# Performance work log

Hardware: AMD Instinct MI355X
Metric: run time of the kernel (lower is better)

The kernel has to match this reference:

```python
import jax, jax.numpy as jnp
import numpy as np

K = 3  # kernel_size
KK = K * K


def conv2d(x, w, b, stride=1, padding=1, dilation=1):
    out = jax.lax.conv_general_dilated(
        x, w, (stride, stride), [(padding, padding), (padding, padding)],
        rhs_dilation=(dilation, dilation),
        dimension_numbers=('NCHW', 'OIHW', 'NCHW'))
    return out + b[None, :, None, None]


def bilinear_gather(x, py, px):
    # x: [B,C,H,W]; py,px: [B,KK,H,W] float sampling coords (zero outside).
    B, C, H, W = x.shape
    y0 = jnp.floor(py)
    x0 = jnp.floor(px)
    wy1 = py - y0
    wx1 = px - x0
    xf = x.reshape(B, C, H * W)

    def corner(yc, xc, wgt):
        valid = (yc >= 0) & (yc <= H - 1) & (xc >= 0) & (xc <= W - 1)
        yi = jnp.clip(yc, 0, H - 1).astype(jnp.int32)
        xi = jnp.clip(xc, 0, W - 1).astype(jnp.int32)
        idx = (yi * W + xi).reshape(B, 1, -1)  # [B,1,KK*H*W]
        v = jnp.take_along_axis(xf, jnp.broadcast_to(idx, (B, C, idx.shape[-1])), axis=2)
        v = v.reshape(B, C, *yc.shape[1:])  # [B,C,KK,H,W]
        return v * (wgt * valid)[:, None]

    return (corner(y0, x0, (1 - wy1) * (1 - wx1)) +
            corner(y0, x0 + 1, (1 - wy1) * wx1) +
            corner(y0 + 1, x0, wy1 * (1 - wx1)) +
            corner(y0 + 1, x0 + 1, wy1 * wx1))


def modulated_deform_conv(x, offset, mask, w, b, stride=1, padding=1, dilation=1):
    B, C, H, W = x.shape
    Ho, Wo = offset.shape[2], offset.shape[3]
    off = offset.reshape(B, KK, 2, Ho, Wo)
    dy, dx = off[:, :, 0], off[:, :, 1]  # [B,KK,Ho,Wo]
    ki, kj = jnp.meshgrid(jnp.arange(K), jnp.arange(K), indexing='ij')
    ki = ki.reshape(-1).astype(x.dtype)  # [KK]
    kj = kj.reshape(-1).astype(x.dtype)
    base_y = (jnp.arange(Ho) * stride - padding).astype(x.dtype)
    base_x = (jnp.arange(Wo) * stride - padding).astype(x.dtype)
    py = base_y[None, None, :, None] + (ki * dilation)[None, :, None, None] + dy
    px = base_x[None, None, None, :] + (kj * dilation)[None, :, None, None] + dx
    x_off = bilinear_gather(x, py, px)              # [B,C,KK,Ho,Wo]
    x_off = x_off * mask[:, None]                   # modulation
    w_flat = w.reshape(w.shape[0], C, KK)           # [O,C,KK]
    out = jnp.einsum('bckhw,ock->bohw', x_off, w_flat)
    return out + b[None, :, None, None]


def setup_inputs() -> dict:
    key = jax.random.key(0)
    ks = jax.random.split(key, 7)
    B, C, O, H, W = 8, 64, 64, 128, 128
    x = jax.random.normal(ks[0], (B, C, H, W), dtype=jnp.float32)
    # offset/mask predictor convs (zero-init in the module; randomized small here
    # so offsets/masks are non-trivial for kernel correctness testing)
    p_w = jax.random.normal(ks[1], (2 * KK, C, 3, 3), dtype=jnp.float32) * 0.02
    p_b = jax.random.normal(ks[2], (2 * KK,), dtype=jnp.float32) * 0.1
    m_w = jax.random.normal(ks[3], (KK, C, 3, 3), dtype=jnp.float32) * 0.02
    m_b = jax.random.normal(ks[4], (KK,), dtype=jnp.float32) * 0.1
    # deformable conv weights
    d_w = jax.random.normal(ks[5], (O, C, K, K), dtype=jnp.float32) * (1.0 / np.sqrt(C * KK))
    d_b = jax.random.normal(ks[6], (O,), dtype=jnp.float32) * 0.01
    return {"x": x, "p_w": p_w, "p_b": p_b, "m_w": m_w, "m_b": m_b, "d_w": d_w, "d_b": d_b}


def reference(x, p_w, p_b, m_w, m_b, d_w, d_b):
    offset = conv2d(x, p_w, p_b, stride=1, padding=1, dilation=1)   # [B,18,H,W]
    mask = jax.nn.sigmoid(conv2d(x, m_w, m_b, stride=1, padding=1, dilation=1))  # [B,9,H,W]
    out = modulated_deform_conv(x, offset, mask, d_w, d_b, stride=1, padding=1, dilation=1)
    return (out, offset)
```

## Files before the change

### kernel.cpp

```cpp
#include <hip/hip_runtime.h>
#include <math.h>

#define KK 9
#define BB 8
#define CC 64
#define OO 64
#define HH 128
#define WW 128
#define HWSZ (HH*WW)

typedef _Float16 half8 __attribute__((ext_vector_type(8)));
typedef float    floatx4 __attribute__((ext_vector_type(4)));

#define WP_ELEMS (9*2*4*32*8)
#define WD_ELEMS (9*2*4*64*8)
#define XH_ELEMS ((size_t)BB*HWSZ*64)
#define NCONV 2048

__global__ __launch_bounds__(256) void prep(
    const float* __restrict__ x,
    const float* __restrict__ p_w, const float* __restrict__ m_w,
    const float* __restrict__ d_w,
    _Float16* __restrict__ Wp, _Float16* __restrict__ Wd, _Float16* __restrict__ x_h,
    int conv_blocks)
{
    const int blk = blockIdx.x;
    const int tid = threadIdx.x;
    if (blk < conv_blocks) {
        __shared__ _Float16 sh[64][72];
        const int b    = blk >> 8;
        const int pix0 = (blk & 255) * 64;
        const float* xb = x + (size_t)b*CC*HWSZ + pix0;
        {
            const int p     = tid & 63;
            const int cbase = tid >> 6;
            #pragma unroll
            for (int j = 0; j < 16; ++j) {
                const int c = j*4 + cbase;
                sh[p][c] = (_Float16)xb[(size_t)c*HWSZ + p];
            }
        }
        __syncthreads();
        {
            const int p  = tid >> 2;
            const int c0 = (tid & 3) * 16;
            _Float16* dst = x_h + ((size_t)b*HWSZ + pix0 + p)*64 + c0;
            *(half8*)dst       = *(const half8*)&sh[p][c0];
            *(half8*)(dst + 8) = *(const half8*)&sh[p][c0 + 8];
        }
    } else {
        const int i = (blk - conv_blocks)*256 + tid;
        if (i < WP_ELEMS) {
            const int e = i & 7, n = (i>>3)&31, quad = (i>>8)&3, ks = (i>>10)&1, k = i>>11;
            const int c = ks*32 + quad*8 + e;
            float v = 0.f;
            if (n < 18)      v = p_w[(n*CC + c)*KK + k];
            else if (n < 27) v = m_w[((n-18)*CC + c)*KK + k];
            Wp[i] = (_Float16)v;
        } else if (i < WP_ELEMS + WD_ELEMS) {
            const int j = i - WP_ELEMS;
            const int e = j & 7, o = (j>>3)&63, quad = (j>>9)&3, ks = (j>>11)&1, k = j>>12;
            const int c = ks*32 + quad*8 + e;
            Wd[j] = (_Float16)d_w[(o*CC + c)*KK + k];
        }
    }
}

__global__ __launch_bounds__(256, 6) void dcn_fused(
    const _Float16* __restrict__ x_h,
    const _Float16* __restrict__ Wp, const _Float16* __restrict__ Wd,
    const float* __restrict__ p_b, const float* __restrict__ m_b,
    const float* __restrict__ db,
    float* __restrict__ out, float* __restrict__ offset_out)
{
    __shared__ alignas(16) float T[27*68];

    const int tid  = threadIdx.x;
    const int wv   = tid >> 6;
    const int lane = tid & 63;
    const int quad = lane >> 4;
    const int l15  = lane & 15;
    const int b    = blockIdx.x & 7;
    const int seg  = blockIdx.x >> 3;
    const int row  = seg >> 1;
    const int col0 = (seg & 1) * 64;
    const int pix0 = row * WW + col0;
    const _Float16* xbh = x_h + (size_t)b*HWSZ*64;

    const int p2   = wv*16 + (lane >> 2);
    const int part = lane & 3;
    const int wx2  = col0 + p2;
    const int bidx = ((l15 << 2) | quad) << 2;

    union U { half8 h; int i[4]; };

    floatx4 accp[2];
    accp[0] = (floatx4)0.f; accp[1] = (floatx4)0.f;
    #pragma unroll
    for (int k = 0; k < 9; ++k) {
        const int hy = row + k/3 - 1;
        const int hx = wx2 + k%3 - 1;
        const bool vld = (hy >= 0) & (hy < HH) & (hx >= 0) & (hx < WW);
        const _Float16* ap = xbh + (size_t)(vld ? hy*WW + hx : 0)*64 + part*8;
        const half8 z = (half8)(_Float16)0.f;
        half8 a0 = *(const half8*)ap;
        half8 a1 = *(const half8*)(ap + 32);
        a0 = vld ? a0 : z;
        a1 = vld ? a1 : z;
        U u0, u1, b0, b1;
        u0.h = a0; u1.h = a1;
        #pragma unroll
        for (int d = 0; d < 4; ++d) {
            b0.i[d] = __builtin_amdgcn_ds_bpermute(bidx, u0.i[d]);
            b1.i[d] = __builtin_amdgcn_ds_bpermute(bidx, u1.i[d]);
        }
        const _Float16* wp = Wp + k*2048 + quad*256 + l15*8;
        accp[0] = __builtin_amdgcn_mfma_f32_16x16x32_f16(b0.h, *(const half8*)(wp),              accp[0], 0, 0, 0);
        accp[1] = __builtin_amdgcn_mfma_f32_16x16x32_f16(b0.h, *(const half8*)(wp + 128),        accp[1], 0, 0, 0);
        accp[0] = __builtin_amdgcn_mfma_f32_16x16x32_f16(b1.h, *(const half8*)(wp + 1024),       accp[0], 0, 0, 0);
        accp[1] = __builtin_amdgcn_mfma_f32_16x16x32_f16(b1.h, *(const half8*)(wp + 1024 + 128), accp[1], 0, 0, 0);
    }

    #pragma unroll
    for (int nt = 0; nt < 2; ++nt) {
        const int ch = nt*16 + l15;
        if (ch < 27) {
            const float bias = (ch < 18) ? p_b[ch] : m_b[ch-18];
            #pragma unroll
            for (int r = 0; r < 4; ++r)
                T[ch*68 + wv*16 + quad*4 + r] = accp[nt][r] + bias;
        }
    }
    __syncthreads();

    {
        float* offp = offset_out + (size_t)b*18*HWSZ + pix0;
        #pragma unroll
        for (int j = 0; j < 5; ++j) {
            const int idx = j*256 + tid;
            if (idx < 18*64) {
                const int ch = idx >> 6, pp = idx & 63;
                offp[ch*HWSZ + pp] = T[ch*68 + pp];
            }
        }
    }
    float dyk[9], dxk[9], mkk[9];
    #pragma unroll
    for (int k = 0; k < 9; ++k) {
        dyk[k] = T[(2*k  )*68 + p2];
        dxk[k] = T[(2*k+1)*68 + p2];
        mkk[k] = 1.f / (1.f + expf(-T[(18+k)*68 + p2]));
    }

    floatx4 acc[4];
    #pragma unroll
    for (int nt = 0; nt < 4; ++nt) acc[nt] = (floatx4)0.f;

    #pragma unroll
    for (int k = 0; k < 9; ++k) {
        const float dy = dyk[k], dx = dxk[k], mk = mkk[k];
        const float py  = (float)(row - 1 + k/3) + dy;
        const float pxf = (float)(wx2 - 1 + k%3) + dx;
        const float y0f = floorf(py), x0f = floorf(pxf);
        const int   iy0 = (int)y0f,   ix0 = (int)x0f;
        const float wy1 = py - y0f,   wx1 = pxf - x0f;
        const float wy0 = 1.f - wy1,  wx0 = 1.f - wx1;
        const bool vy0 = ((unsigned)iy0     < (unsigned)HH);
        const bool vy1 = ((unsigned)(iy0+1) < (unsigned)HH);
        const bool vx0 = ((unsigned)ix0     < (unsigned)WW);
        const bool vx1 = ((unsigned)(ix0+1) < (unsigned)WW);
        const int cy0 = min(max(iy0,   0), HH-1), cy1 = min(max(iy0+1, 0), HH-1);
        const int cx0 = min(max(ix0,   0), WW-1), cx1 = min(max(ix0+1, 0), WW-1);
        const int i0 = cy0*WW+cx0, i1 = cy0*WW+cx1, i2 = cy1*WW+cx0, i3 = cy1*WW+cx1;
        const _Float16 g0 = (_Float16)(wy0*wx0*((vy0&vx0) ? mk : 0.f));
        const _Float16 g1 = (_Float16)(wy0*wx1*((vy0&vx1) ? mk : 0.f));
        const _Float16 g2 = (_Float16)(wy1*wx0*((vy1&vx0) ? mk : 0.f));
        const _Float16 g3 = (_Float16)(wy1*wx1*((vy1&vx1) ? mk : 0.f));

        const _Float16* c0p = xbh + (size_t)i0*64 + part*8;
        const _Float16* c1p = xbh + (size_t)i1*64 + part*8;
        const _Float16* c2p = xbh + (size_t)i2*64 + part*8;
        const _Float16* c3p = xbh + (size_t)i3*64 + part*8;
        const half8 p0l = *(const half8*)c0p, p0h = *(const half8*)(c0p + 32);
        const half8 p1l = *(const half8*)c1p, p1h = *(const half8*)(c1p + 32);
        const half8 p2l = *(const half8*)c2p, p2h = *(const half8*)(c2p + 32);
        const half8 p3l = *(const half8*)c3p, p3h = *(const half8*)(c3p + 32);
        const half8 lo = p0l*g0 + p1l*g1 + p2l*g2 + p3l*g3;
        const half8 hi = p0h*g0 + p1h*g1 + p2h*g2 + p3h*g3;

        U ulo, uhi, a0u, a1u;
        ulo.h = lo; uhi.h = hi;
        #pragma unroll
        for (int d = 0; d < 4; ++d) {
            a0u.i[d] = __builtin_amdgcn_ds_bpermute(bidx, ulo.i[d]);
            a1u.i[d] = __builtin_amdgcn_ds_bpermute(bidx, uhi.i[d]);
        }

        #pragma unroll
        for (int ks = 0; ks < 2; ++ks) {
            const half8 af = ks ? a1u.h : a0u.h;
            const _Float16* wdp = Wd + k*4096 + ks*2048 + quad*512 + l15*8;
            #pragma unroll
            for (int nt = 0; nt < 4; ++nt)
                acc[nt] = __builtin_amdgcn_mfma_f32_16x16x32_f16(af, *(const half8*)(wdp + nt*128), acc[nt], 0, 0, 0);
        }
    }

    __syncthreads();
    float* T2 = T;
    #pragma unroll
    for (int oc = 0; oc < 4; ++oc) {
        #pragma unroll
        for (int r = 0; r < 4; ++r)
            T2[l15*68 + wv*16 + quad*4 + r] = acc[oc][r];
        __syncthreads();
        #pragma unroll
        for (int j = 0; j < 4; ++j) {
            const int idx = j*256 + tid;
            const int o16 = idx >> 6, pp = idx & 63;
            out[((size_t)b*OO + oc*16 + o16)*HWSZ + pix0 + pp] = T2[o16*68 + pp] + db[oc*16 + o16];
        }
        __syncthreads();
    }
}

__global__ __launch_bounds__(256, 4) void dcn_fused_lds(
    const float* __restrict__ x,
    const _Float16* __restrict__ Wp, const _Float16* __restrict__ Wd,
    const float* __restrict__ p_b, const float* __restrict__ m_b,
    const float* __restrict__ db,
    float* __restrict__ out, float* __restrict__ offset_out)
{
    __shared__ alignas(16) _Float16 A_sh[128][72];
    __shared__ alignas(16) _Float16 WM_sh[32*72];
    __shared__ alignas(16) _Float16 Wd_sh[64][72];

    const int tid   = threadIdx.x;
    const int wv    = tid >> 6;
    const int lane  = tid & 63;
    const int quad  = lane >> 4;
    const int l15   = lane & 15;
    const int b     = blockIdx.x & 7;
    const int row   = blockIdx.x >> 3;
    const int pix0  = row * WW;
    const int p     = tid & 127;
    const int chalf = (tid >> 7) * 32;
    const int h = row, w = p;
    const float* xb = x + (size_t)b*CC*HWSZ;
    _Float16 (*W_sh)[72] = (_Float16 (*)[72])WM_sh;

    floatx4 accp[2][2];
    #pragma unroll
    for (int mt = 0; mt < 2; ++mt)
        #pragma unroll
        for (int nt = 0; nt < 2; ++nt) accp[mt][nt] = (floatx4)0.f;

    for (int k = 0; k < 9; ++k) {
        {
            const int n  = tid >> 3;
            const int c0 = (tid & 7) * 8;
            *(half8*)&W_sh[n][c0] =
                *(const half8*)(Wp + k*2048 + (c0>>5)*1024 + ((c0>>3)&3)*256 + n*8);
        }
        const int hy = h + (k/3) - 1;
        const int wx = w + (k%3) - 1;
        const bool vld = (hy >= 0) & (hy < HH) & (wx >= 0) & (wx < WW);
        const float* xs = xb + hy*WW + wx;
        #pragma unroll
        for (int cb = 0; cb < 4; ++cb) {
            union { half8 v; _Float16 e[8]; } u;
            #pragma unroll
            for (int j = 0; j < 8; ++j)
                u.e[j] = (_Float16)(vld ? xs[(size_t)(chalf + cb*8 + j)*HWSZ] : 0.f);
            *(half8*)&A_sh[p][chalf + cb*8] = u.v;
        }
        __syncthreads();
        #pragma unroll
        for (int ks = 0; ks < 2; ++ks) {
            half8 bf[2];
            #pragma unroll
            for (int nt = 0; nt < 2; ++nt)
                bf[nt] = *(const half8*)&W_sh[nt*16 + l15][ks*32 + quad*8];
            #pragma unroll
            for (int mt = 0; mt < 2; ++mt) {
                half8 af = *(const half8*)&A_sh[wv*32 + mt*16 + l15][ks*32 + quad*8];
                accp[mt][0] = __builtin_amdgcn_mfma_f32_16x16x32_f16(af, bf[0], accp[mt][0], 0, 0, 0);
                accp[mt][1] = __builtin_amdgcn_mfma_f32_16x16x32_f16(af, bf[1], accp[mt][1], 0, 0, 0);
            }
        }
        __syncthreads();
    }

    float (*T)[132] = (float (*)[132])&A_sh[0][0];
    #pragma unroll
    for (int nt = 0; nt < 2; ++nt) {
        const int ch = nt*16 + l15;
        if (ch < 27) {
            #pragma unroll
            for (int mt = 0; mt < 2; ++mt)
                #pragma unroll
                for (int r = 0; r < 4; ++r)
                    T[ch][wv*32 + mt*16 + quad*4 + r] = accp[mt][nt][r];
        }
    }
    __syncthreads();

    float dyk[9], dxk[9], mkk[9];
    float* offp = offset_out + (size_t)b*18*HWSZ + pix0;
    #pragma unroll
    for (int k = 0; k < 9; ++k) {
        dyk[k] = T[2*k][p]   + p_b[2*k];
        dxk[k] = T[2*k+1][p] + p_b[2*k+1];
        mkk[k] = 1.f / (1.f + expf(-(T[18+k][p] + m_b[k])));
    }
    if (tid < 128) {
        #pragma unroll
        for (int k = 0; k < 9; ++k) {
            offp[(2*k  )*HWSZ + p] = dyk[k];
            offp[(2*k+1)*HWSZ + p] = dxk[k];
        }
    }
    __syncthreads();

    floatx4 acc[2][4];
    #pragma unroll
    for (int mt = 0; mt < 2; ++mt)
        #pragma unroll
        for (int nt = 0; nt < 4; ++nt) acc[mt][nt] = (floatx4)0.f;

    for (int k = 0; k < 9; ++k) {
        {
            const int o  = tid >> 2;
            const int c0 = (tid & 3) * 16;
            *(half8*)&Wd_sh[o][c0] =
                *(const half8*)(Wd + k*4096 + (c0>>5)*2048 + ((c0>>3)&3)*512 + o*8);
            const int c8 = c0 + 8;
            *(half8*)&Wd_sh[o][c8] =
                *(const half8*)(Wd + k*4096 + (c8>>5)*2048 + ((c8>>3)&3)*512 + o*8);
        }
        const float mk = mkk[k];
        const float py = (float)(h - 1 + k/3) + dyk[k];
        const float px = (float)(w - 1 + k%3) + dxk[k];
        const float y0f = floorf(py), x0f = floorf(px);
        const int   iy0 = (int)y0f,   ix0 = (int)x0f;
        const float wy1 = py - y0f,   wx1 = px - x0f;
        const float wy0 = 1.f - wy1,  wx0 = 1.f - wx1;
        const bool vy0 = (iy0   >= 0) & (iy0   < HH);
        const bool vy1 = (iy0+1 >= 0) & (iy0+1 < HH);
        const bool vx0 = (ix0   >= 0) & (ix0   < WW);
        const bool vx1 = (ix0+1 >= 0) & (ix0+1 < WW);
        const int cy0 = min(max(iy0,   0), HH-1), cy1 = min(max(iy0+1, 0), HH-1);
        const int cx0 = min(max(ix0,   0), WW-1), cx1 = min(max(ix0+1, 0), WW-1);
        const int i0 = cy0*WW+cx0; const float w0 = wy0*wx0*((vy0&vx0) ? mk : 0.f);
        const int i1 = cy0*WW+cx1; const float w1 = wy0*wx1*((vy0&vx1) ? mk : 0.f);
        const int i2 = cy1*WW+cx0; const float w2 = wy1*wx0*((vy1&vx0) ? mk : 0.f);
        const int i3 = cy1*WW+cx1; const float w3 = wy1*wx1*((vy1&vx1) ? mk : 0.f);
        #pragma unroll
        for (int cb = 0; cb < 4; ++cb) {
            union { half8 v; _Float16 e[8]; } u;
            #pragma unroll
            for (int j = 0; j < 8; ++j) {
                const float* xc = xb + (size_t)(chalf + cb*8 + j)*HWSZ;
                u.e[j] = (_Float16)(w0*xc[i0] + w1*xc[i1] + w2*xc[i2] + w3*xc[i3]);
            }
            *(half8*)&A_sh[p][chalf + cb*8] = u.v;
        }
        __syncthreads();
        #pragma unroll
        for (int ks = 0; ks < 2; ++ks) {
            half8 bf[4];
            #pragma unroll
            for (int nt = 0; nt < 4; ++nt)
                bf[nt] = *(const half8*)&Wd_sh[nt*16 + l15][ks*32 + quad*8];
            #pragma unroll
            for (int mt = 0; mt < 2; ++mt) {
                half8 af = *(const half8*)&A_sh[wv*32 + mt*16 + l15][ks*32 + quad*8];
                #pragma unroll
                for (int nt = 0; nt < 4; ++nt)
                    acc[mt][nt] = __builtin_amdgcn_mfma_f32_16x16x32_f16(af, bf[nt], acc[mt][nt], 0, 0, 0);
            }
        }
        __syncthreads();
    }

    float (*T2)[132] = (float (*)[132])&A_sh[0][0];
    #pragma unroll
    for (int oc = 0; oc < 4; ++oc) {
        #pragma unroll
        for (int mt = 0; mt < 2; ++mt)
            #pragma unroll
            for (int r = 0; r < 4; ++r)
                T2[l15][wv*32 + mt*16 + quad*4 + r] = acc[mt][oc][r];
        __syncthreads();
        #pragma unroll
        for (int j = 0; j < 8; ++j) {
            const int idx = tid + j*256;
            const int o16 = idx >> 7, pp = idx & 127;
            out[((size_t)b*OO + oc*16 + o16)*HWSZ + pix0 + pp] = T2[o16][pp] + db[oc*16 + o16];
        }
        __syncthreads();
    }
}

extern "C" void kernel_launch(void* const* d_in, const int* in_sizes, int n_in,
                              void* d_out, int out_size, void* d_ws, size_t ws_size,
                              hipStream_t stream) {
    const float* x   = (const float*)d_in[0];
    const float* p_w = (const float*)d_in[1];
    const float* p_b = (const float*)d_in[2];
    const float* m_w = (const float*)d_in[3];
    const float* m_b = (const float*)d_in[4];
    const float* dw  = (const float*)d_in[5];
    const float* db  = (const float*)d_in[6];

    float* out        = (float*)d_out;
    float* offset_out = out + (size_t)BB*OO*HWSZ;

    _Float16* Wp  = (_Float16*)d_ws;
    _Float16* Wd  = Wp + WP_ELEMS;
    _Float16* x_h = Wd + WD_ELEMS;

    const int nrep = (WP_ELEMS + WD_ELEMS + 255) / 256;
    const size_t need = (size_t)(WP_ELEMS + WD_ELEMS + XH_ELEMS) * sizeof(_Float16);
    if (ws_size >= need) {
        prep<<<dim3(NCONV + nrep), 256, 0, stream>>>(x, p_w, m_w, dw, Wp, Wd, x_h, NCONV);
        dcn_fused<<<dim3(256*BB), 256, 0, stream>>>(x_h, Wp, Wd, p_b, m_b, db, out, offset_out);
    } else {
        prep<<<dim3(nrep), 256, 0, stream>>>(x, p_w, m_w, dw, Wp, Wd, x_h, 0);
        dcn_fused_lds<<<dim3(128*BB), 256, 0, stream>>>(x, Wp, Wd, p_b, m_b, db, out, offset_out);
    }
}
```

Measured before the change: 159.7 us.

## Stage conv weights in LDS and split deform loop over channel halves

Copies the predictor weights and then each channel half of the deform-conv weights into a 36KB shared-memory buffer, so MFMA B operands come from LDS instead of repeated global loads. The deform loop is restructured to run twice over the 9 taps, once per 32-channel half, so only one half of the weights needs to be resident at a time. This recomputes the bilinear coordinates and weights twice and cuts register pressure. The occupancy hint drops from 6 to 3 blocks per CU because of the added shared memory, and extra barriers are added around each weight reload.

```diff
diff --git a/kernel.cpp b/kernel.cpp
--- a/kernel.cpp
+++ b/kernel.cpp
@@ -66,14 +66,15 @@
     }
 }
 
-__global__ __launch_bounds__(256, 6) void dcn_fused(
+__global__ __launch_bounds__(256, 3) void dcn_fused(
     const _Float16* __restrict__ x_h,
     const _Float16* __restrict__ Wp, const _Float16* __restrict__ Wd,
     const float* __restrict__ p_b, const float* __restrict__ m_b,
     const float* __restrict__ db,
     float* __restrict__ out, float* __restrict__ offset_out)
 {
-    __shared__ alignas(16) float T[27*68];
+    __shared__ alignas(16) _Float16 WL[9*2048];
+    __shared__ alignas(16) float    T[27*68];
 
     const int tid  = threadIdx.x;
     const int wv   = tid >> 6;
@@ -93,6 +94,13 @@
     const int bidx = ((l15 << 2) | quad) << 2;
 
     union U { half8 h; int i[4]; };
+
+    #pragma unroll
+    for (int j = 0; j < 9; ++j) {
+        const int c = j*256 + tid;
+        *(half8*)&WL[c*8] = *(const half8*)(Wp + c*8);
+    }
+    __syncthreads();
 
     floatx4 accp[2];
     accp[0] = (floatx4)0.f; accp[1] = (floatx4)0.f;
@@ -114,7 +122,7 @@
             b0.i[d] = __builtin_amdgcn_ds_bpermute(bidx, u0.i[d]);
             b1.i[d] = __builtin_amdgcn_ds_bpermute(bidx, u1.i[d]);
         }
-        const _Float16* wp = Wp + k*2048 + quad*256 + l15*8;
+        const _Float16* wp = &WL[k*2048 + quad*256 + l15*8];
         accp[0] = __builtin_amdgcn_mfma_f32_16x16x32_f16(b0.h, *(const half8*)(wp),              accp[0], 0, 0, 0);
         accp[1] = __builtin_amdgcn_mfma_f32_16x16x32_f16(b0.h, *(const half8*)(wp + 128),        accp[1], 0, 0, 0);
         accp[0] = __builtin_amdgcn_mfma_f32_16x16x32_f16(b1.h, *(const half8*)(wp + 1024),       accp[0], 0, 0, 0);
@@ -156,53 +164,58 @@
     #pragma unroll
     for (int nt = 0; nt < 4; ++nt) acc[nt] = (floatx4)0.f;
 
-    #pragma unroll
-    for (int k = 0; k < 9; ++k) {
-        const float dy = dyk[k], dx = dxk[k], mk = mkk[k];
-        const float py  = (float)(row - 1 + k/3) + dy;
-        const float pxf = (float)(wx2 - 1 + k%3) + dx;
-        const float y0f = floorf(py), x0f = floorf(pxf);
-        const int   iy0 = (int)y0f,   ix0 = (int)x0f;
-        const float wy1 = py - y0f,   wx1 = pxf - x0f;
-        const float wy0 = 1.f - wy1,  wx0 = 1.f - wx1;
-        const bool vy0 = ((unsigned)iy0     < (unsigned)HH);
-        const bool vy1 = ((unsigned)(iy0+1) < (unsigned)HH);
-        const bool vx0 = ((unsigned)ix0     < (unsigned)WW);
-        const bool vx1 = ((unsigned)(ix0+1) < (unsigned)WW);
-        const int cy0 = min(max(iy0,   0), HH-1), cy1 = min(max(iy0+1, 0), HH-1);
-        const int cx0 = min(max(ix0,   0), WW-1), cx1 = min(max(ix0+1, 0), WW-1);
-        const int i0 = cy0*WW+cx0, i1 = cy0*WW+cx1, i2 = cy1*WW+cx0, i3 = cy1*WW+cx1;
-        const _Float16 g0 = (_Float16)(wy0*wx0*((vy0&vx0) ? mk : 0.f));
-        const _Float16 g1 = (_Float16)(wy0*wx1*((vy0&vx1) ? mk : 0.f));
-        const _Float16 g2 = (_Float16)(wy1*wx0*((vy1&vx0) ? mk : 0.f));
-        const _Float16 g3 = (_Float16)(wy1*wx1*((vy1&vx1) ? mk : 0.f));
-
-        const _Float16* c0p = xbh + (size_t)i0*64 + part*8;
-        const _Float16* c1p = xbh + (size_t)i1*64 + part*8;
-        const _Float16* c2p = xbh + (size_t)i2*64 + part*8;
-        const _Float16* c3p = xbh + (size_t)i3*64 + part*8;
-        const half8 p0l = *(const half8*)c0p, p0h = *(const half8*)(c0p + 32);
-        const half8 p1l = *(const half8*)c1p, p1h = *(const half8*)(c1p + 32);
-        const half8 p2l = *(const half8*)c2p, p2h = *(const half8*)(c2p + 32);
-        const half8 p3l = *(const half8*)c3p, p3h = *(const half8*)(c3p + 32);
-        const half8 lo = p0l*g0 + p1l*g1 + p2l*g2 + p3l*g3;
-        const half8 hi = p0h*g0 + p1h*g1 + p2h*g2 + p3h*g3;
-
-        U ulo, uhi, a0u, a1u;
-        ulo.h = lo; uhi.h = hi;
-        #pragma unroll
-        for (int d = 0; d < 4; ++d) {
-            a0u.i[d] = __builtin_amdgcn_ds_bpermute(bidx, ulo.i[d]);
-            a1u.i[d] = __builtin_amdgcn_ds_bpermute(bidx, uhi.i[d]);
-        }
-
-        #pragma unroll
-        for (int ks = 0; ks < 2; ++ks) {
-            const half8 af = ks ? a1u.h : a0u.h;
-            const _Float16* wdp = Wd + k*4096 + ks*2048 + quad*512 + l15*8;
+    for (int ks = 0; ks < 2; ++ks) {
+        __syncthreads();
+        #pragma unroll
+        for (int j = 0; j < 9; ++j) {
+            const int c   = j*256 + tid;
+            const int kk  = c >> 8;
+            const int rem = c & 255;
+            *(half8*)&WL[kk*2048 + rem*8] = *(const half8*)(Wd + kk*4096 + ks*2048 + rem*8);
+        }
+        __syncthreads();
+
+        #pragma unroll
+        for (int k = 0; k < 9; ++k) {
+            const float dy = dyk[k], dx = dxk[k], mk = mkk[k];
+            const float py  = (float)(row - 1 + k/3) + dy;
+            const float pxf = (float)(wx2 - 1 + k%3) + dx;
+            const float y0f = floorf(py), x0f = floorf(pxf);
+            const int   iy0 = (int)y0f,   ix0 = (int)x0f;
+            const float wy1 = py - y0f,   wx1 = pxf - x0f;
+            const float wy0 = 1.f - wy1,  wx0 = 1.f - wx1;
+            const bool vy0 = ((unsigned)iy0     < (unsigned)HH);
+            const bool vy1 = ((unsigned)(iy0+1) < (unsigned)HH);
+            const bool vx0 = ((unsigned)ix0     < (unsigned)WW);
+            const bool vx1 = ((unsigned)(ix0+1) < (unsigned)WW);
+            const int cy0 = min(max(iy0,   0), HH-1), cy1 = min(max(iy0+1, 0), HH-1);
+            const int cx0 = min(max(ix0,   0), WW-1), cx1 = min(max(ix0+1, 0), WW-1);
+            const int i0 = cy0*WW+cx0, i1 = cy0*WW+cx1, i2 = cy1*WW+cx0, i3 = cy1*WW+cx1;
+            const _Float16 g0 = (_Float16)(wy0*wx0*((vy0&vx0) ? mk : 0.f));
+            const _Float16 g1 = (_Float16)(wy0*wx1*((vy0&vx1) ? mk : 0.f));
+            const _Float16 g2 = (_Float16)(wy1*wx0*((vy1&vx0) ? mk : 0.f));
+            const _Float16 g3 = (_Float16)(wy1*wx1*((vy1&vx1) ? mk : 0.f));
+
+            const _Float16* c0p = xbh + (size_t)i0*64 + ks*32 + part*8;
+            const _Float16* c1p = xbh + (size_t)i1*64 + ks*32 + part*8;
+            const _Float16* c2p = xbh + (size_t)i2*64 + ks*32 + part*8;
+            const _Float16* c3p = xbh + (size_t)i3*64 + ks*32 + part*8;
+            const half8 q0 = *(const half8*)c0p;
+            const half8 q1 = *(const half8*)c1p;
+            const half8 q2 = *(const half8*)c2p;
+            const half8 q3 = *(const half8*)c3p;
+            const half8 lo = q0*g0 + q1*g1 + q2*g2 + q3*g3;
+
+            U ulo, au;
+            ulo.h = lo;
+            #pragma unroll
+            for (int d = 0; d < 4; ++d)
+                au.i[d] = __builtin_amdgcn_ds_bpermute(bidx, ulo.i[d]);
+
+            const _Float16* wdp = &WL[k*2048 + quad*512 + l15*8];
             #pragma unroll
             for (int nt = 0; nt < 4; ++nt)
-                acc[nt] = __builtin_amdgcn_mfma_f32_16x16x32_f16(af, *(const half8*)(wdp + nt*128), acc[nt], 0, 0, 0);
+                acc[nt] = __builtin_amdgcn_mfma_f32_16x16x32_f16(au.h, *(const half8*)(wdp + nt*128), acc[nt], 0, 0, 0);
         }
     }
 
```

Result: slower. 315.3 us (+97.4%).
